# Performance work log

Measured on AMD Instinct MI355X. Metric: run time of the kernel, lower is better.

Reference implementation:

```python
import jax, jax.numpy as jnp
import numpy as np

N_NODES = 100000


def gcn_conv(x, W, b, src, dst, n):
    # PyG GCNConv: linear transform, add self-loops, symmetric degree normalization,
    # scatter-add aggregation from src -> dst, then bias.
    h = x @ W  # [N, F_out]
    loop = jnp.arange(n, dtype=src.dtype)
    s = jnp.concatenate([src, loop])  # sources incl. self-loops
    d = jnp.concatenate([dst, loop])  # targets incl. self-loops
    deg = jax.ops.segment_sum(jnp.ones_like(d, dtype=h.dtype), d, num_segments=n)
    dinv = jnp.where(deg > 0, jax.lax.rsqrt(deg), 0.0)
    norm = dinv[s] * dinv[d]  # [E+N]
    msg = h[s] * norm[:, None]  # gather + scale
    out = jax.ops.segment_sum(msg, d, num_segments=n)  # scatter-add
    return out + b


def setup_inputs() -> dict:
    key = jax.random.key(0)
    k1, k2, k3, k4 = jax.random.split(key, 4)
    n, e = N_NODES, 1600000
    z = jax.random.normal(k1, (n, 64), dtype=jnp.float32)
    edge_index = jax.random.randint(k2, (2, e), 0, n, dtype=jnp.int64)
    # Glorot-ish init for weights, zero bias (PyG default bias init is zeros)
    W1 = jax.random.normal(k3, (64, 128), dtype=jnp.float32) * (1.0 / np.sqrt(64))
    b1 = jnp.zeros((128,), dtype=jnp.float32)
    W2 = jax.random.normal(k4, (128, 64), dtype=jnp.float32) * (1.0 / np.sqrt(128))
    b2 = jnp.zeros((64,), dtype=jnp.float32)
    return {"z": z, "edge_index": edge_index, "W1": W1, "b1": b1, "W2": W2, "b2": b2}


def reference(z, edge_index, W1, b1, W2, b2):
    n = z.shape[0]
    src, dst = edge_index[0], edge_index[1]
    h = gcn_conv(z, W1, b1, src, dst, n)
    h = jax.nn.relu(h)
    x_hat = gcn_conv(h, W2, b2, src, dst, n)
    return x_hat
```

## Files before the change

kernel.cpp:

```cpp
#include <hip/hip_runtime.h>
#include <hip/hip_bf16.h>


#define WAVE 64
#define BSHIFT 8
#define NPB 256
#define CAP 5120
#define CH 4096
#define NBMAX 512

typedef __attribute__((ext_vector_type(8))) short bf16x8;
typedef __attribute__((ext_vector_type(4))) float f32x4;

__device__ inline float bf16_to_f32(unsigned short h) {
    return __uint_as_float(((unsigned int)h) << 16);
}
__device__ inline unsigned short f32_to_bf16(float f) {
    unsigned int x = __float_as_uint(f);
    return (unsigned short)((x + 0x7FFFu + ((x >> 16) & 1u)) >> 16);
}

__global__ void prep(const float* __restrict__ W1, const float* __restrict__ W2,
                     unsigned short* __restrict__ W1t, unsigned short* __restrict__ W2t,
                     int* __restrict__ bcursor, int NB)
{
    int i = blockIdx.x * blockDim.x + threadIdx.x;
    if (i < NB) bcursor[i] = 0;
    if (i < 128 * 64) {
        int n = i >> 6, k = i & 63;
        W1t[i] = f32_to_bf16(W1[k * 128 + n]);
    }
    if (i < 64 * 128) {
        int n = i >> 7, k = i & 127;
        W2t[i] = f32_to_bf16(W2[k * 64 + n]);
    }
}

__global__ __launch_bounds__(256) void bin_edges(
        const int* __restrict__ src, const int* __restrict__ dst,
        int* __restrict__ bcursor, int2* __restrict__ ebuf, int E, int NB)
{
    __shared__ int hist[NBMAX];
    __shared__ int cur[NBMAX];
    const int t  = threadIdx.x;
    const int e0 = blockIdx.x * CH;

    for (int b = t; b < NB; b += 256) hist[b] = 0;
    __syncthreads();

#pragma unroll
    for (int j = 0; j < CH / 256; ++j) {
        int e = e0 + j * 256 + t;
        if (e < E) atomicAdd(&hist[dst[e] >> BSHIFT], 1);
    }
    __syncthreads();

    for (int b = t; b < NB; b += 256) {
        int c = hist[b];
        cur[b] = (c > 0) ? atomicAdd(&bcursor[b], c) : 0;
    }
    __syncthreads();

#pragma unroll
    for (int j = 0; j < CH / 256; ++j) {
        int e = e0 + j * 256 + t;
        if (e < E) {
            int s = src[e], d = dst[e];
            int b = d >> BSHIFT;
            int pos = atomicAdd(&cur[b], 1);
            ebuf[(size_t)b * CAP + pos] = make_int2(s, d);
        }
    }
}

__global__ __launch_bounds__(256) void build_csr(
        const int2* __restrict__ ebuf, const int* __restrict__ bcursor,
        const float* __restrict__ z, float* __restrict__ dinv,
        int* __restrict__ rbeg, int* __restrict__ rend,
        int* __restrict__ csr, unsigned short* __restrict__ u, int N)
{
    __shared__ int   h[NPB];
    __shared__ int   tmp[NPB];
    __shared__ float sdv[NPB];
    const int t   = threadIdx.x;
    const int b   = blockIdx.x;
    const int n0  = b << BSHIFT;
    const int cnt = bcursor[b];
    const size_t base = (size_t)b * CAP;

    h[t] = 0;
    __syncthreads();

    for (int i = t; i < cnt; i += 256)
        atomicAdd(&h[ebuf[base + i].y - n0], 1);
    __syncthreads();

    int deg = h[t];
    tmp[t] = deg;
    __syncthreads();
    for (int off = 1; off < 256; off <<= 1) {
        int x = (t >= off) ? tmp[t - off] : 0;
        __syncthreads();
        tmp[t] += x;
        __syncthreads();
    }
    int st = tmp[t] - deg;

    int node = n0 + t;
    float di = rsqrtf((float)deg + 1.0f);
    sdv[t] = di;
    if (node < N) {
        dinv[node] = di;
        rbeg[node] = (int)base + st;
        rend[node] = (int)base + st + deg;
    }
    h[t] = st;
    __syncthreads();

    for (int i = t; i < cnt; i += 256) {
        int2 e = ebuf[base + i];
        int p = atomicAdd(&h[e.y - n0], 1);
        csr[base + p] = e.x;
    }

    const int nloc = (N - n0 < NPB) ? (N - n0) : NPB;
    for (int i = t; i < nloc * 16; i += 256) {
        int r = i >> 4, kq = i & 15;
        float d2 = sdv[r];
        float4 v = ((const float4*)(z + (size_t)(n0 + r) * 64))[kq];
        ushort4 o;
        o.x = f32_to_bf16(v.x * d2);
        o.y = f32_to_bf16(v.y * d2);
        o.z = f32_to_bf16(v.z * d2);
        o.w = f32_to_bf16(v.w * d2);
        ((ushort4*)(u + (size_t)(n0 + r) * 64))[kq] = o;
    }
}

template<bool POST>
__global__ __launch_bounds__(256) void aggregate64_bf16(
        const unsigned short* __restrict__ hs, const int* __restrict__ rbeg,
        const int* __restrict__ rend, const int* __restrict__ csr,
        const float* __restrict__ dinv, const float* __restrict__ b,
        void* __restrict__ out_, int N)
{
    int node = (int)((blockIdx.x * (size_t)blockDim.x + threadIdx.x) >> 6);
    int lane = threadIdx.x & 63;
    if (node >= N) return;
    node = __builtin_amdgcn_readfirstlane(node);

    const int beg = rbeg[node];
    const int end = rend[node];

    float acc = bf16_to_f32(hs[(size_t)node * 64 + lane]);

    int e = beg;
    for (; e + 16 <= end; e += 16) {
        int s[16];
#pragma unroll
        for (int j = 0; j < 16; ++j) s[j] = csr[e + j];
        float v[16];
#pragma unroll
        for (int j = 0; j < 16; ++j) v[j] = bf16_to_f32(hs[(size_t)s[j] * 64 + lane]);
        float t0 = ((v[0] + v[1]) + (v[2] + v[3])) + ((v[4] + v[5]) + (v[6] + v[7]));
        float t1 = ((v[8] + v[9]) + (v[10] + v[11])) + ((v[12] + v[13]) + (v[14] + v[15]));
        acc += t0 + t1;
    }
    for (; e + 4 <= end; e += 4) {
        int s0 = csr[e+0], s1 = csr[e+1], s2 = csr[e+2], s3 = csr[e+3];
        float v0 = bf16_to_f32(hs[(size_t)s0 * 64 + lane]);
        float v1 = bf16_to_f32(hs[(size_t)s1 * 64 + lane]);
        float v2 = bf16_to_f32(hs[(size_t)s2 * 64 + lane]);
        float v3 = bf16_to_f32(hs[(size_t)s3 * 64 + lane]);
        acc += (v0 + v1) + (v2 + v3);
    }
    for (; e < end; ++e)
        acc += bf16_to_f32(hs[(size_t)csr[e] * 64 + lane]);

    if (POST) {
        float o = dinv[node] * acc + b[lane];
        ((float*)out_)[(size_t)node * 64 + lane] = o;
    } else {
        ((unsigned short*)out_)[(size_t)node * 64 + lane] = f32_to_bf16(acc);
    }
}

#define TILE 32
#define W1T_ST 72
#define W2T_ST 136
#define A_ST   72
#define X1_ST  136

__global__ __launch_bounds__(256) void gemm12_mfma(
        const unsigned short* __restrict__ agg1,
        const unsigned short* __restrict__ W1t,
        const float* __restrict__ b1,
        const unsigned short* __restrict__ W2t,
        const float* __restrict__ dinv,
        unsigned short* __restrict__ hs2, int N)
{
    __shared__ unsigned short sW1[128 * W1T_ST];
    __shared__ unsigned short sW2[64 * W2T_ST];
    __shared__ unsigned short sA[TILE * A_ST];
    __shared__ unsigned short sX[TILE * X1_ST];
    __shared__ float sdv[TILE];

    const int tid  = threadIdx.x;
    const int row0 = blockIdx.x * TILE;
    const int lane = tid & 63;
    const int wv   = tid >> 6;
    const int l16  = lane & 15;
    const int quad = lane >> 4;

    for (int i = tid; i < 128 * 8; i += 256) {
        int r = i >> 3, c = i & 7;
        *(uint4*)&sW1[r * W1T_ST + c * 8] = *(const uint4*)&W1t[r * 64 + c * 8];
    }
    for (int i = tid; i < 64 * 16; i += 256) {
        int r = i >> 4, c = i & 15;
        *(uint4*)&sW2[r * W2T_ST + c * 8] = *(const uint4*)&W2t[r * 128 + c * 8];
    }
    for (int i = tid; i < TILE * 8; i += 256) {
        int r = i >> 3, c = i & 7;
        int gr = row0 + r;
        uint4 v = make_uint4(0u, 0u, 0u, 0u);
        if (gr < N) v = *(const uint4*)&agg1[(size_t)gr * 64 + c * 8];
        *(uint4*)&sA[r * A_ST + c * 8] = v;
    }
    if (tid < TILE) {
        int gr = row0 + tid;
        sdv[tid] = (gr < N) ? dinv[gr] : 0.0f;
    }
    __syncthreads();

    {
        const int mt  = wv & 1;
        const int ntb = (wv >> 1) * 4;
        f32x4 acc[4];
#pragma unroll
        for (int t = 0; t < 4; ++t) acc[t] = (f32x4)0.0f;

#pragma unroll
        for (int k0 = 0; k0 < 64; k0 += 32) {
            bf16x8 af = *(const bf16x8*)&sA[(mt * 16 + l16) * A_ST + k0 + quad * 8];
#pragma unroll
            for (int t = 0; t < 4; ++t) {
                bf16x8 bf = *(const bf16x8*)&sW1[((ntb + t) * 16 + l16) * W1T_ST + k0 + quad * 8];
                acc[t] = __builtin_amdgcn_mfma_f32_16x16x32_bf16(af, bf, acc[t], 0, 0, 0);
            }
        }

#pragma unroll
        for (int t = 0; t < 4; ++t) {
            int col = (ntb + t) * 16 + l16;
            float bb = b1[col];
#pragma unroll
            for (int r = 0; r < 4; ++r) {
                int lr = mt * 16 + quad * 4 + r;
                float o = fmaxf(acc[t][r] * sdv[lr] + bb, 0.0f);
                sX[lr * X1_ST + col] = f32_to_bf16(o);
            }
        }
    }
    __syncthreads();

    {
        const int mt  = wv & 1;
        const int ntb = (wv >> 1) * 2;
        f32x4 acc[2];
#pragma unroll
        for (int t = 0; t < 2; ++t) acc[t] = (f32x4)0.0f;

#pragma unroll
        for (int k0 = 0; k0 < 128; k0 += 32) {
            bf16x8 af = *(const bf16x8*)&sX[(mt * 16 + l16) * X1_ST + k0 + quad * 8];
#pragma unroll
            for (int t = 0; t < 2; ++t) {
                bf16x8 bf = *(const bf16x8*)&sW2[((ntb + t) * 16 + l16) * W2T_ST + k0 + quad * 8];
                acc[t] = __builtin_amdgcn_mfma_f32_16x16x32_bf16(af, bf, acc[t], 0, 0, 0);
            }
        }

#pragma unroll
        for (int t = 0; t < 2; ++t) {
            int col = (ntb + t) * 16 + l16;
#pragma unroll
            for (int r = 0; r < 4; ++r) {
                int lr = mt * 16 + quad * 4 + r;
                int gr = row0 + lr;
                if (gr < N)
                    hs2[(size_t)gr * 64 + col] = f32_to_bf16(acc[t][r] * sdv[lr]);
            }
        }
    }
}

static inline size_t align_up(size_t x, size_t a) { return (x + a - 1) / a * a; }

extern "C" void kernel_launch(void* const* d_in, const int* in_sizes, int n_in,
                              void* d_out, int out_size, void* d_ws, size_t ws_size,
                              hipStream_t stream) {
    const float* z    = (const float*)d_in[0];
    const int*   eidx = (const int*)d_in[1];
    const float* W1   = (const float*)d_in[2];
    const float* b1   = (const float*)d_in[3];
    const float* W2   = (const float*)d_in[4];
    const float* b2   = (const float*)d_in[5];
    float* out = (float*)d_out;

    const int N = in_sizes[0] / 64;
    const int E = in_sizes[1] / 2;
    const int* src = eidx;
    const int* dst = eidx + E;
    const int NB = (N + NPB - 1) >> BSHIFT;

    char* ws = (char*)d_ws;
    size_t off = 0;
    float* dinv    = (float*)(ws + off); off = align_up(off + (size_t)N * 4, 512);
    int*   rbeg    = (int*)  (ws + off); off = align_up(off + (size_t)N * 4, 512);
    int*   rend    = (int*)  (ws + off); off = align_up(off + (size_t)N * 4, 512);
    int*   bcursor = (int*)  (ws + off); off = align_up(off + (size_t)NBMAX * 4, 512);
    unsigned short* W1t = (unsigned short*)(ws + off); off = align_up(off + 8192 * 2, 512);
    unsigned short* W2t = (unsigned short*)(ws + off); off = align_up(off + 8192 * 2, 512);
    int*   csr     = (int*)  (ws + off); off = align_up(off + (size_t)NB * CAP * 4, 512);
    float* bufA    = (float*)(ws + off); off = align_up(off + (size_t)N * 64 * 4, 512);
    float* bufB    = (float*)(ws + off); off = align_up(off + (size_t)N * 64 * 4, 512);
    float* bufC    = (float*)(ws + off); off = align_up(off + (size_t)N * 128 * 4, 512);
    int2*  ebuf    = (int2*)bufC;
    (void)ws_size;

    unsigned short* u    = (unsigned short*)bufA;
    unsigned short* agg1 = (unsigned short*)bufB;
    unsigned short* hs2  = (unsigned short*)bufA;

    prep<<<32, 256, 0, stream>>>(W1, W2, W1t, W2t, bcursor, NB);

    bin_edges<<<(E + CH - 1) / CH, 256, 0, stream>>>(src, dst, bcursor, ebuf, E, NB);
    build_csr<<<NB, 256, 0, stream>>>(ebuf, bcursor, z, dinv, rbeg, rend, csr, u, N);

    aggregate64_bf16<false><<<(N + 3) / 4, 256, 0, stream>>>(u, rbeg, rend, csr, dinv, nullptr, agg1, N);

    gemm12_mfma<<<(N + TILE - 1) / TILE, 256, 0, stream>>>(agg1, W1t, b1, W2t, dinv, hs2, N);

    aggregate64_bf16<true><<<(N + 3) / 4, 256, 0, stream>>>(hs2, rbeg, rend, csr, dinv, b2, out, N);
}
```

Baseline: 241.9 us.

## Fuse first aggregation into GEMM kernel and split edge buffer into SoA

```diff
diff --git a/kernel.cpp b/kernel.cpp
--- a/kernel.cpp
+++ b/kernel.cpp
@@ -20,6 +20,35 @@
     return (unsigned short)((x + 0x7FFFu + ((x >> 16) & 1u)) >> 16);
 }
 
+__device__ inline float gather_rows(const unsigned short* __restrict__ hs,
+                                    const int* __restrict__ csr,
+                                    int beg, int end, int lane, float acc)
+{
+    int e = beg;
+    for (; e + 16 <= end; e += 16) {
+        int s[16];
+#pragma unroll
+        for (int j = 0; j < 16; ++j) s[j] = csr[e + j];
+        float v[16];
+#pragma unroll
+        for (int j = 0; j < 16; ++j) v[j] = bf16_to_f32(hs[(size_t)s[j] * 64 + lane]);
+        float t0 = ((v[0] + v[1]) + (v[2] + v[3])) + ((v[4] + v[5]) + (v[6] + v[7]));
+        float t1 = ((v[8] + v[9]) + (v[10] + v[11])) + ((v[12] + v[13]) + (v[14] + v[15]));
+        acc += t0 + t1;
+    }
+    for (; e + 4 <= end; e += 4) {
+        int s0 = csr[e+0], s1 = csr[e+1], s2 = csr[e+2], s3 = csr[e+3];
+        float v0 = bf16_to_f32(hs[(size_t)s0 * 64 + lane]);
+        float v1 = bf16_to_f32(hs[(size_t)s1 * 64 + lane]);
+        float v2 = bf16_to_f32(hs[(size_t)s2 * 64 + lane]);
+        float v3 = bf16_to_f32(hs[(size_t)s3 * 64 + lane]);
+        acc += (v0 + v1) + (v2 + v3);
+    }
+    for (; e < end; ++e)
+        acc += bf16_to_f32(hs[(size_t)csr[e] * 64 + lane]);
+    return acc;
+}
+
 __global__ void prep(const float* __restrict__ W1, const float* __restrict__ W2,
                      unsigned short* __restrict__ W1t, unsigned short* __restrict__ W2t,
                      int* __restrict__ bcursor, int NB)
@@ -38,7 +67,8 @@
 
 __global__ __launch_bounds__(256) void bin_edges(
         const int* __restrict__ src, const int* __restrict__ dst,
-        int* __restrict__ bcursor, int2* __restrict__ ebuf, int E, int NB)
+        int* __restrict__ bcursor, int* __restrict__ esrc,
+        unsigned char* __restrict__ edloc, int E, int NB)
 {
     __shared__ int hist[NBMAX];
     __shared__ int cur[NBMAX];
@@ -65,16 +95,20 @@
     for (int j = 0; j < CH / 256; ++j) {
         int e = e0 + j * 256 + t;
         if (e < E) {
-            int s = src[e], d = dst[e];
+            int s = __builtin_nontemporal_load(&src[e]);
+            int d = dst[e];
             int b = d >> BSHIFT;
             int pos = atomicAdd(&cur[b], 1);
-            ebuf[(size_t)b * CAP + pos] = make_int2(s, d);
+            size_t idx = (size_t)b * CAP + pos;
+            esrc[idx]  = s;
+            edloc[idx] = (unsigned char)(d & (NPB - 1));
         }
     }
 }
 
 __global__ __launch_bounds__(256) void build_csr(
-        const int2* __restrict__ ebuf, const int* __restrict__ bcursor,
+        const int* __restrict__ esrc, const unsigned char* __restrict__ edloc,
+        const int* __restrict__ bcursor,
         const float* __restrict__ z, float* __restrict__ dinv,
         int* __restrict__ rbeg, int* __restrict__ rend,
         int* __restrict__ csr, unsigned short* __restrict__ u, int N)
@@ -92,7 +126,7 @@
     __syncthreads();
 
     for (int i = t; i < cnt; i += 256)
-        atomicAdd(&h[ebuf[base + i].y - n0], 1);
+        atomicAdd(&h[edloc[base + i]], 1);
     __syncthreads();
 
     int deg = h[t];
@@ -118,70 +152,23 @@
     __syncthreads();
 
     for (int i = t; i < cnt; i += 256) {
-        int2 e = ebuf[base + i];
-        int p = atomicAdd(&h[e.y - n0], 1);
-        csr[base + p] = e.x;
+        int dl = edloc[base + i];
+        int p = atomicAdd(&h[dl], 1);
+        csr[base + p] = __builtin_nontemporal_load(&esrc[base + i]);
     }
 
     const int nloc = (N - n0 < NPB) ? (N - n0) : NPB;
     for (int i = t; i < nloc * 16; i += 256) {
         int r = i >> 4, kq = i & 15;
         float d2 = sdv[r];
-        float4 v = ((const float4*)(z + (size_t)(n0 + r) * 64))[kq];
+        const f32x4* zr = (const f32x4*)(z + (size_t)(n0 + r) * 64);
+        f32x4 v = __builtin_nontemporal_load(zr + kq);
         ushort4 o;
-        o.x = f32_to_bf16(v.x * d2);
-        o.y = f32_to_bf16(v.y * d2);
-        o.z = f32_to_bf16(v.z * d2);
-        o.w = f32_to_bf16(v.w * d2);
+        o.x = f32_to_bf16(v[0] * d2);
+        o.y = f32_to_bf16(v[1] * d2);
+        o.z = f32_to_bf16(v[2] * d2);
+        o.w = f32_to_bf16(v[3] * d2);
         ((ushort4*)(u + (size_t)(n0 + r) * 64))[kq] = o;
-    }
-}
-
-template<bool POST>
-__global__ __launch_bounds__(256) void aggregate64_bf16(
-        const unsigned short* __restrict__ hs, const int* __restrict__ rbeg,
-        const int* __restrict__ rend, const int* __restrict__ csr,
-        const float* __restrict__ dinv, const float* __restrict__ b,
-        void* __restrict__ out_, int N)
-{
-    int node = (int)((blockIdx.x * (size_t)blockDim.x + threadIdx.x) >> 6);
-    int lane = threadIdx.x & 63;
-    if (node >= N) return;
-    node = __builtin_amdgcn_readfirstlane(node);
-
-    const int beg = rbeg[node];
-    const int end = rend[node];
-
-    float acc = bf16_to_f32(hs[(size_t)node * 64 + lane]);
-
-    int e = beg;
-    for (; e + 16 <= end; e += 16) {
-        int s[16];
-#pragma unroll
-        for (int j = 0; j < 16; ++j) s[j] = csr[e + j];
-        float v[16];
-#pragma unroll
-        for (int j = 0; j < 16; ++j) v[j] = bf16_to_f32(hs[(size_t)s[j] * 64 + lane]);
-        float t0 = ((v[0] + v[1]) + (v[2] + v[3])) + ((v[4] + v[5]) + (v[6] + v[7]));
-        float t1 = ((v[8] + v[9]) + (v[10] + v[11])) + ((v[12] + v[13]) + (v[14] + v[15]));
-        acc += t0 + t1;
-    }
-    for (; e + 4 <= end; e += 4) {
-        int s0 = csr[e+0], s1 = csr[e+1], s2 = csr[e+2], s3 = csr[e+3];
-        float v0 = bf16_to_f32(hs[(size_t)s0 * 64 + lane]);
-        float v1 = bf16_to_f32(hs[(size_t)s1 * 64 + lane]);
-        float v2 = bf16_to_f32(hs[(size_t)s2 * 64 + lane]);
-        float v3 = bf16_to_f32(hs[(size_t)s3 * 64 + lane]);
-        acc += (v0 + v1) + (v2 + v3);
-    }
-    for (; e < end; ++e)
-        acc += bf16_to_f32(hs[(size_t)csr[e] * 64 + lane]);
-
-    if (POST) {
-        float o = dinv[node] * acc + b[lane];
-        ((float*)out_)[(size_t)node * 64 + lane] = o;
-    } else {
-        ((unsigned short*)out_)[(size_t)node * 64 + lane] = f32_to_bf16(acc);
     }
 }
 
@@ -191,8 +178,10 @@
 #define A_ST   72
 #define X1_ST  136
 
-__global__ __launch_bounds__(256) void gemm12_mfma(
-        const unsigned short* __restrict__ agg1,
+__global__ __launch_bounds__(512, 6) void agg_gemm12(
+        const unsigned short* __restrict__ u,
+        const int* __restrict__ rbeg, const int* __restrict__ rend,
+        const int* __restrict__ csr,
         const unsigned short* __restrict__ W1t,
         const float* __restrict__ b1,
         const unsigned short* __restrict__ W2t,
@@ -212,46 +201,52 @@
     const int l16  = lane & 15;
     const int quad = lane >> 4;
 
-    for (int i = tid; i < 128 * 8; i += 256) {
+    for (int i = tid; i < 128 * 8; i += 512) {
         int r = i >> 3, c = i & 7;
         *(uint4*)&sW1[r * W1T_ST + c * 8] = *(const uint4*)&W1t[r * 64 + c * 8];
     }
-    for (int i = tid; i < 64 * 16; i += 256) {
+    for (int i = tid; i < 64 * 16; i += 512) {
         int r = i >> 4, c = i & 15;
         *(uint4*)&sW2[r * W2T_ST + c * 8] = *(const uint4*)&W2t[r * 128 + c * 8];
-    }
-    for (int i = tid; i < TILE * 8; i += 256) {
-        int r = i >> 3, c = i & 7;
-        int gr = row0 + r;
-        uint4 v = make_uint4(0u, 0u, 0u, 0u);
-        if (gr < N) v = *(const uint4*)&agg1[(size_t)gr * 64 + c * 8];
-        *(uint4*)&sA[r * A_ST + c * 8] = v;
     }
     if (tid < TILE) {
         int gr = row0 + tid;
         sdv[tid] = (gr < N) ? dinv[gr] : 0.0f;
     }
+
+#pragma unroll
+    for (int r = 0; r < 4; ++r) {
+        int lr = wv * 4 + r;
+        int node = __builtin_amdgcn_readfirstlane(row0 + lr);
+        float acc = 0.0f;
+        if (node < N) {
+            const int beg = rbeg[node];
+            const int end = rend[node];
+            acc = bf16_to_f32(u[(size_t)node * 64 + lane]);
+            acc = gather_rows(u, csr, beg, end, lane, acc);
+        }
+        sA[lr * A_ST + lane] = f32_to_bf16(acc);
+    }
     __syncthreads();
 
     {
         const int mt  = wv & 1;
-        const int ntb = (wv >> 1) * 4;
-        f32x4 acc[4];
-#pragma unroll
-        for (int t = 0; t < 4; ++t) acc[t] = (f32x4)0.0f;
+        const int ntb = (wv >> 1) * 2;
+        f32x4 acc[2];
+        acc[0] = (f32x4)0.0f; acc[1] = (f32x4)0.0f;
 
 #pragma unroll
         for (int k0 = 0; k0 < 64; k0 += 32) {
             bf16x8 af = *(const bf16x8*)&sA[(mt * 16 + l16) * A_ST + k0 + quad * 8];
 #pragma unroll
-            for (int t = 0; t < 4; ++t) {
+            for (int t = 0; t < 2; ++t) {
                 bf16x8 bf = *(const bf16x8*)&sW1[((ntb + t) * 16 + l16) * W1T_ST + k0 + quad * 8];
                 acc[t] = __builtin_amdgcn_mfma_f32_16x16x32_bf16(af, bf, acc[t], 0, 0, 0);
             }
         }
 
 #pragma unroll
-        for (int t = 0; t < 4; ++t) {
+        for (int t = 0; t < 2; ++t) {
             int col = (ntb + t) * 16 + l16;
             float bb = b1[col];
 #pragma unroll
@@ -265,34 +260,49 @@
     __syncthreads();
 
     {
-        const int mt  = wv & 1;
-        const int ntb = (wv >> 1) * 2;
-        f32x4 acc[2];
-#pragma unroll
-        for (int t = 0; t < 2; ++t) acc[t] = (f32x4)0.0f;
+        const int mt = wv & 1;
+        const int nt = wv >> 1;
+        f32x4 acc = (f32x4)0.0f;
 
 #pragma unroll
         for (int k0 = 0; k0 < 128; k0 += 32) {
             bf16x8 af = *(const bf16x8*)&sX[(mt * 16 + l16) * X1_ST + k0 + quad * 8];
-#pragma unroll
-            for (int t = 0; t < 2; ++t) {
-                bf16x8 bf = *(const bf16x8*)&sW2[((ntb + t) * 16 + l16) * W2T_ST + k0 + quad * 8];
-                acc[t] = __builtin_amdgcn_mfma_f32_16x16x32_bf16(af, bf, acc[t], 0, 0, 0);
+            bf16x8 bf = *(const bf16x8*)&sW2[(nt * 16 + l16) * W2T_ST + k0 + quad * 8];
+            acc = __builtin_amdgcn_mfma_f32_16x16x32_bf16(af, bf, acc, 0, 0, 0);
+        }
+
+        int col = nt * 16 + l16;
+#pragma unroll
+        for (int r = 0; r < 4; ++r) {
+            int lr = mt * 16 + quad * 4 + r;
+            int gr = row0 + lr;
+            if (gr < N) {
+                unsigned short hv = f32_to_bf16(acc[r] * sdv[lr]);
+                __builtin_nontemporal_store(hv, &hs2[(size_t)gr * 64 + col]);
             }
         }
-
-#pragma unroll
-        for (int t = 0; t < 2; ++t) {
-            int col = (ntb + t) * 16 + l16;
-#pragma unroll
-            for (int r = 0; r < 4; ++r) {
-                int lr = mt * 16 + quad * 4 + r;
-                int gr = row0 + lr;
-                if (gr < N)
-                    hs2[(size_t)gr * 64 + col] = f32_to_bf16(acc[t][r] * sdv[lr]);
-            }
-        }
-    }
+    }
+}
+
+__global__ __launch_bounds__(256) void aggregate_post(
+        const unsigned short* __restrict__ hs, const int* __restrict__ rbeg,
+        const int* __restrict__ rend, const int* __restrict__ csr,
+        const float* __restrict__ dinv, const float* __restrict__ b,
+        float* __restrict__ out, int N)
+{
+    int node = (int)((blockIdx.x * (size_t)blockDim.x + threadIdx.x) >> 6);
+    int lane = threadIdx.x & 63;
+    if (node >= N) return;
+    node = __builtin_amdgcn_readfirstlane(node);
+
+    const int beg = rbeg[node];
+    const int end = rend[node];
+
+    float acc = bf16_to_f32(hs[(size_t)node * 64 + lane]);
+    acc = gather_rows(hs, csr, beg, end, lane, acc);
+
+    float o = dinv[node] * acc + b[lane];
+    __builtin_nontemporal_store(o, &out[(size_t)node * 64 + lane]);
 }
 
 static inline size_t align_up(size_t x, size_t a) { return (x + a - 1) / a * a; }
@@ -326,21 +336,20 @@
     float* bufA    = (float*)(ws + off); off = align_up(off + (size_t)N * 64 * 4, 512);
     float* bufB    = (float*)(ws + off); off = align_up(off + (size_t)N * 64 * 4, 512);
     float* bufC    = (float*)(ws + off); off = align_up(off + (size_t)N * 128 * 4, 512);
-    int2*  ebuf    = (int2*)bufC;
     (void)ws_size;
 
     unsigned short* u    = (unsigned short*)bufA;
-    unsigned short* agg1 = (unsigned short*)bufB;
-    unsigned short* hs2  = (unsigned short*)bufA;
+    unsigned short* hs2  = (unsigned short*)bufB;
+    int*            esrc  = (int*)bufC;
+    unsigned char*  edloc = (unsigned char*)((char*)bufC + (size_t)NB * CAP * 4);
 
     prep<<<32, 256, 0, stream>>>(W1, W2, W1t, W2t, bcursor, NB);
 
-    bin_edges<<<(E + CH - 1) / CH, 256, 0, stream>>>(src, dst, bcursor, ebuf, E, NB);
-    build_csr<<<NB, 256, 0, stream>>>(ebuf, bcursor, z, dinv, rbeg, rend, csr, u, N);
-
-    aggregate64_bf16<false><<<(N + 3) / 4, 256, 0, stream>>>(u, rbeg, rend, csr, dinv, nullptr, agg1, N);
-
-    gemm12_mfma<<<(N + TILE - 1) / TILE, 256, 0, stream>>>(agg1, W1t, b1, W2t, dinv, hs2, N);
-
-    aggregate64_bf16<true><<<(N + 3) / 4, 256, 0, stream>>>(hs2, rbeg, rend, csr, dinv, b2, out, N);
-}
+    bin_edges<<<(E + CH - 1) / CH, 256, 0, stream>>>(src, dst, bcursor, esrc, edloc, E, NB);
+    build_csr<<<NB, 256, 0, stream>>>(esrc, edloc, bcursor, z, dinv, rbeg, rend, csr, u, N);
+
+    agg_gemm12<<<(N + TILE - 1) / TILE, 512, 0, stream>>>(
+        u, rbeg, rend, csr, W1t, b1, W2t, dinv, hs2, N);
+
+    aggregate_post<<<(N + 3) / 4, 256, 0, stream>>>(hs2, rbeg, rend, csr, dinv, b2, out, N);
+}
```

Result: slower. 272.1 us (+12.5%).
